# Kernel tuning notes

Measured on AMD Instinct MI355X. Metric: run time of the kernel, lower is better.

## Reference

```python
import jax, jax.numpy as jnp
import numpy as np

N_NODES = 50000
N_EDGES = 800000
H_DIM = 128
N_REL = 40
N_BASES = 4


def setup_inputs() -> dict:
    key = jax.random.key(0)
    ks = jax.random.split(key, 9)
    h = jax.random.normal(ks[0], (N_NODES, H_DIM), jnp.float32)
    norm = jax.random.uniform(ks[1], (N_EDGES, 1), jnp.float32)
    basis_w = jax.random.normal(ks[2], (N_BASES, H_DIM, H_DIM), jnp.float32) * 0.05
    w_comp = jax.random.normal(ks[3], (N_REL, N_BASES), jnp.float32) * 0.5
    loop_w = jax.random.normal(ks[4], (H_DIM, H_DIM), jnp.float32) * 0.05
    bias = jax.random.normal(ks[5], (H_DIM,), jnp.float32) * 0.05
    src = jax.random.randint(ks[6], (N_EDGES,), 0, N_NODES, jnp.int32)
    dst = jax.random.randint(ks[7], (N_EDGES,), 0, N_NODES, jnp.int32)
    etype = jax.random.randint(ks[8], (N_EDGES,), 0, N_REL, jnp.int32)
    return {"h": h, "norm": norm, "basis_w": basis_w, "w_comp": w_comp,
            "loop_w": loop_w, "bias": bias, "src": src, "dst": dst, "etype": etype}


def reference(h, norm, basis_w, w_comp, loop_w, bias, src, dst, etype):
    # RelGraphConv with 'basis' regularizer, one layer (num_hidden_layers=1):
    #   W_r = sum_b w_comp[r, b] * basis_w[b]
    #   m_e = (h[src_e] @ W_{etype_e}) * norm_e
    #   agg[v] = sum_{e: dst_e = v} m_e
    #   out = relu(agg + bias + h @ loop_w)   (dropout = 0)
    # Contraction reordered for memory efficiency: scatter-add per-basis
    # scaled source features first (node-level), then apply small basis GEMMs.
    n = h.shape[0]
    n_bases = basis_w.shape[0]
    coeff = w_comp[etype] * norm          # [E, B] per-edge basis coefficients * norm
    h_src = h[src]                        # [E, D] edge-gathered source features
    agg = jnp.zeros((n, basis_w.shape[2]), dtype=h.dtype)
    for b in range(n_bases):              # small fixed loop over bases
        s_b = jax.ops.segment_sum(coeff[:, b:b + 1] * h_src, dst, num_segments=n)  # [N, D]
        agg = agg + s_b @ basis_w[b]
    return jax.nn.relu(agg + bias + h @ loop_w)
```

## Files before the change

kernel.cpp:

```cpp
#include <hip/hip_runtime.h>
#include <stdint.h>

#define N_NODES 50000
#define N_EDGES 800000
#define H_DIM 128
#define N_REL 40
#define N_BASES 4
#define N_RANGES 196
#define EP_BLOCKS 200
#define EDGES_PER_BLK 4000
#define STAGE_CAP 5120

typedef __attribute__((ext_vector_type(8))) short bf16x8;
typedef __attribute__((ext_vector_type(4))) float f32x4;

__device__ __forceinline__ unsigned short f2bf(float f) {
    unsigned int u = __float_as_uint(f);
    unsigned int r = u + 0x7fffu + ((u >> 16) & 1u);
    return (unsigned short)(r >> 16);
}

__global__ __launch_bounds__(256) void prep_kernel(
        const float* __restrict__ h,
        const float* __restrict__ basis_w, const float* __restrict__ loop_w,
        const int* __restrict__ src, const int* __restrict__ dst,
        const int* __restrict__ etype, const float* __restrict__ norm,
        unsigned short* __restrict__ A, unsigned short* __restrict__ wt3,
        uint2* __restrict__ pkd, int* __restrict__ gcnt) {
    int bid = blockIdx.x;
    if (bid < 3125) {
        int t = bid * 256 + threadIdx.x;
        int row = t >> 4;
        int cb = (t & 15) * 8;
        const float* p = h + (size_t)row * 128 + cb;
        float4 a0 = ((const float4*)p)[0];
        float4 a1 = ((const float4*)p)[1];
        bf16x8 o;
        o[0] = (short)f2bf(a0.x); o[1] = (short)f2bf(a0.y);
        o[2] = (short)f2bf(a0.z); o[3] = (short)f2bf(a0.w);
        o[4] = (short)f2bf(a1.x); o[5] = (short)f2bf(a1.y);
        o[6] = (short)f2bf(a1.z); o[7] = (short)f2bf(a1.w);
        *(bf16x8*)(A + (size_t)row * H_DIM + cb) = o;
    } else if (bid < 3130) {
        int mat = bid - 3125;
        const float* srcm = (mat < 4) ? (basis_w + mat * 16384) : loop_w;
        int koff = (mat < 4) ? (128 + mat * 128) : 0;
        int t = threadIdx.x;
#pragma unroll
        for (int i = 0; i < 16; ++i) {
            int f = t + i * 256;
            int k = f >> 5;
            int j4 = (f & 31) * 4;
            float4 v = ((const float4*)srcm)[f];
            int kg = koff + k;
            int ks = kg >> 5;
            int quad = (kg >> 3) & 3;
            int jj = kg & 7;
            float vv[4] = {v.x, v.y, v.z, v.w};
#pragma unroll
            for (int d = 0; d < 4; ++d) {
                int j = j4 + d;
                int cg = j >> 4;
                int n16 = j & 15;
                wt3[(size_t)((ks * 8 + cg) * 64 + quad * 16 + n16) * 8 + jj] =
                    f2bf(vv[d]);
            }
        }
    } else {
        __shared__ int lhist[N_RANGES];
        int blk = bid - 3130;
        int t = threadIdx.x;
        if (t < N_RANGES) lhist[t] = 0;
        __syncthreads();
        int e0 = blk * EDGES_PER_BLK;
        for (int i = t; i < EDGES_PER_BLK; i += 256) {
            int e = e0 + i;
            int d = dst[e];
            unsigned int nbf = f2bf(norm[e]);
            pkd[e] = make_uint2((unsigned)src[e] | ((unsigned)etype[e] << 20),
                                (unsigned)d | (nbf << 17));
            atomicAdd(&lhist[d >> 8], 1);
        }
        __syncthreads();
        if (t < N_RANGES) gcnt[t * EP_BLOCKS + blk] = lhist[t];
    }
}

__global__ __launch_bounds__(256) void bucket_scan_a(
        const int* __restrict__ gcnt, int* __restrict__ blkbase,
        int* __restrict__ btot, unsigned* __restrict__ sorted_src,
        float4* __restrict__ sorted_cf) {
    __shared__ int wsum[4];
    int r = blockIdx.x;
    int t = threadIdx.x, lane = t & 63, w = t >> 6;
    if (r == 0 && t < 16) {
        sorted_src[N_EDGES + t] = 0u;
        sorted_cf[N_EDGES + t] = make_float4(0.f, 0.f, 0.f, 0.f);
    }
    int x = (t < EP_BLOCKS) ? gcnt[r * EP_BLOCKS + t] : 0;
    int v = x;
#pragma unroll
    for (int d = 1; d < 64; d <<= 1) {
        int y = __shfl_up(v, d);
        if (lane >= d) v += y;
    }
    if (lane == 63) wsum[w] = v;
    __syncthreads();
    int wpre = 0;
    if (w > 0) wpre += wsum[0];
    if (w > 1) wpre += wsum[1];
    if (w > 2) wpre += wsum[2];
    if (t < EP_BLOCKS) blkbase[r * EP_BLOCKS + t] = wpre + v - x;
    if (t == 255) btot[r] = wpre + v;
}

__global__ __launch_bounds__(256) void binscatter(
        const uint2* __restrict__ pkd, const int* __restrict__ blkbase,
        const int* __restrict__ btot, uint2* __restrict__ bucketed) {
    __shared__ int lcur[N_RANGES];
    __shared__ int wsum[4];
    int t = threadIdx.x, lane = t & 63, w = t >> 6;
    int x = (t < N_RANGES) ? btot[t] : 0;
    int v = x;
#pragma unroll
    for (int d = 1; d < 64; d <<= 1) {
        int y = __shfl_up(v, d);
        if (lane >= d) v += y;
    }
    if (lane == 63) wsum[w] = v;
    __syncthreads();
    int wpre = 0;
    if (w > 0) wpre += wsum[0];
    if (w > 1) wpre += wsum[1];
    if (w > 2) wpre += wsum[2];
    if (t < N_RANGES)
        lcur[t] = (wpre + v - x) + blkbase[t * EP_BLOCKS + blockIdx.x];
    __syncthreads();
    int e0 = blockIdx.x * EDGES_PER_BLK;
    for (int i = t; i < EDGES_PER_BLK; i += 256) {
        uint2 p = pkd[e0 + i];
        int r = (p.y & 0x1FFFF) >> 8;
        int pos = atomicAdd(&lcur[r], 1);
        bucketed[pos] = p;
    }
}

__global__ __launch_bounds__(256) void bucket_sort(
        const int* __restrict__ btot, const uint2* __restrict__ bucketed,
        const float* __restrict__ w_comp,
        unsigned* __restrict__ sorted_src, float4* __restrict__ sorted_cf,
        int* __restrict__ offs) {
    __shared__ int hist[256];
    __shared__ int cur[256];
    __shared__ int wsum[4];
    __shared__ int sbeg;
    __shared__ uint2 stage[STAGE_CAP];
    int r = blockIdx.x;
    int t = threadIdx.x, lane = t & 63, w = t >> 6;
    int x = (t < N_RANGES) ? btot[t] : 0;
    int v = x;
#pragma unroll
    for (int d = 1; d < 64; d <<= 1) {
        int y = __shfl_up(v, d);
        if (lane >= d) v += y;
    }
    if (lane == 63) wsum[w] = v;
    hist[t] = 0;
    __syncthreads();
    int wpre = 0;
    if (w > 0) wpre += wsum[0];
    if (w > 1) wpre += wsum[1];
    if (w > 2) wpre += wsum[2];
    if (t == r) sbeg = wpre + v - x;
    __syncthreads();
    int begin = sbeg;
    int end = begin + btot[r];
    int n = end - begin;
    for (int i = begin + t; i < end; i += 256)
        atomicAdd(&hist[bucketed[i].y & 255], 1);
    __syncthreads();
    int x2 = hist[t];
    int v2 = x2;
#pragma unroll
    for (int d = 1; d < 64; d <<= 1) {
        int y = __shfl_up(v2, d);
        if (lane >= d) v2 += y;
    }
    if (lane == 63) wsum[w] = v2;
    __syncthreads();
    int wpre2 = 0;
    if (w > 0) wpre2 += wsum[0];
    if (w > 1) wpre2 += wsum[1];
    if (w > 2) wpre2 += wsum[2];
    int excl_rel = wpre2 + v2 - x2;
    int node = r * 256 + t;
    if (node < N_NODES) offs[node] = begin + excl_rel;
    if (r == N_RANGES - 1 && t == 0) offs[N_NODES] = N_EDGES;
    cur[t] = excl_rel;
    __syncthreads();
    if (n <= STAGE_CAP) {
        for (int i = begin + t; i < end; i += 256) {
            uint2 p = bucketed[i];
            int pos = atomicAdd(&cur[p.y & 255], 1);
            stage[pos] = make_uint2(p.x, (p.y >> 17) << 16);
        }
        __syncthreads();
        for (int i = t; i < n; i += 256) {
            uint2 p = stage[i];
            float nm = __uint_as_float(p.y);
            float4 wc = ((const float4*)w_comp)[p.x >> 20];
            sorted_src[begin + i] = p.x & 0xFFFFF;
            sorted_cf[begin + i] =
                make_float4(wc.x * nm, wc.y * nm, wc.z * nm, wc.w * nm);
        }
    } else {
        for (int i = begin + t; i < end; i += 256) {
            uint2 p = bucketed[i];
            int pos = atomicAdd(&cur[p.y & 255], 1);
            float nm = __uint_as_float((p.y >> 17) << 16);
            float4 wc = ((const float4*)w_comp)[p.x >> 20];
            sorted_src[begin + pos] = p.x & 0xFFFFF;
            sorted_cf[begin + pos] =
                make_float4(wc.x * nm, wc.y * nm, wc.z * nm, wc.w * nm);
        }
    }
}

__global__ __launch_bounds__(512, 8) void agg_gemm(
        const int* __restrict__ offs, const unsigned* __restrict__ ssrc,
        const float4* __restrict__ scf,
        const unsigned short* __restrict__ Ab,
        const unsigned short* __restrict__ wt3,
        const float* __restrict__ bias, float* __restrict__ out) {
    __shared__ __align__(16) unsigned short S[32 * 640];
    int wv = threadIdx.x >> 6;
    int lane = threadIdx.x & 63;
    int nbase = blockIdx.x * 32;
    const unsigned int* Au = (const unsigned int*)Ab;

#pragma unroll
    for (int q = 0; q < 4; ++q) {
        int row = (wv << 2) + q;
        int v = __builtin_amdgcn_readfirstlane(nbase + row);
        float a0l = 0.f, a0h = 0.f, a1l = 0.f, a1h = 0.f;
        float a2l = 0.f, a2h = 0.f, a3l = 0.f, a3h = 0.f;
        unsigned int hb = 0u;
        if (v < N_NODES) {
            hb = Au[(size_t)v * 64 + lane];
            int begin = __builtin_amdgcn_readfirstlane(offs[v]);
            int end   = __builtin_amdgcn_readfirstlane(offs[v + 1]);
            for (int j = begin; j < end; j += 8) {
                int rem = end - j;
                unsigned su[8];
                float4 c[8];
#pragma unroll
                for (int k = 0; k < 8; ++k) su[k] = ssrc[j + k];
#pragma unroll
                for (int k = 0; k < 8; ++k) c[k] = scf[j + k];
                if (rem < 8) {
#pragma unroll
                    for (int k = 0; k < 8; ++k)
                        if (k >= rem) {
                            su[k] = 0u;
                            c[k] = make_float4(0.f, 0.f, 0.f, 0.f);
                        }
                }
                unsigned u[8];
#pragma unroll
                for (int k = 0; k < 8; ++k)
                    u[k] = Au[(size_t)su[k] * 64 + lane];
#pragma unroll
                for (int k = 0; k < 8; ++k) {
                    float lo = __uint_as_float(u[k] << 16);
                    float hi = __uint_as_float(u[k] & 0xffff0000u);
                    a0l += c[k].x * lo; a0h += c[k].x * hi;
                    a1l += c[k].y * lo; a1h += c[k].y * hi;
                    a2l += c[k].z * lo; a2h += c[k].z * hi;
                    a3l += c[k].w * lo; a3h += c[k].w * hi;
                }
            }
        }
        char* rp = (char*)S + row * 1280;
        int swz = (row & 7) << 4;
        *(unsigned int*)(rp + ((lane * 4) ^ swz)) = hb;
        *(unsigned int*)(rp + ((256 + lane * 4) ^ swz)) =
            (unsigned int)f2bf(a0l) | ((unsigned int)f2bf(a0h) << 16);
        *(unsigned int*)(rp + ((512 + lane * 4) ^ swz)) =
            (unsigned int)f2bf(a1l) | ((unsigned int)f2bf(a1h) << 16);
        *(unsigned int*)(rp + ((768 + lane * 4) ^ swz)) =
            (unsigned int)f2bf(a2l) | ((unsigned int)f2bf(a2h) << 16);
        *(unsigned int*)(rp + ((1024 + lane * 4) ^ swz)) =
            (unsigned int)f2bf(a3l) | ((unsigned int)f2bf(a3h) << 16);
    }
    __syncthreads();

    int n16 = lane & 15;
    int quad = lane >> 4;
    f32x4 acc0 = (f32x4)0.f, acc1 = (f32x4)0.f;

    const char* s0p = (const char*)S + n16 * 1280;
    const char* s1p = s0p + 16 * 1280;
    int swz2 = (n16 & 7) << 4;
    const unsigned short* bwp = wt3 + (size_t)wv * 512 + (size_t)lane * 8;

#pragma unroll
    for (int ks = 0; ks < 20; ++ks) {
        int off = (ks * 64 + quad * 16) ^ swz2;
        bf16x8 a0 = *(const bf16x8*)(s0p + off);
        bf16x8 a1 = *(const bf16x8*)(s1p + off);
        bf16x8 b  = *(const bf16x8*)(bwp + (size_t)ks * 4096);
        acc0 = __builtin_amdgcn_mfma_f32_16x16x32_bf16(a0, b, acc0, 0, 0, 0);
        acc1 = __builtin_amdgcn_mfma_f32_16x16x32_bf16(a1, b, acc1, 0, 0, 0);
    }

    int col = (wv << 4) + n16;
    float bv = bias[col];
#pragma unroll
    for (int rg = 0; rg < 4; ++rg) {
        int r0 = nbase + quad * 4 + rg;
        if (r0 < N_NODES)
            out[(size_t)r0 * H_DIM + col] = fmaxf(acc0[rg] + bv, 0.f);
        int r1 = nbase + 16 + quad * 4 + rg;
        if (r1 < N_NODES)
            out[(size_t)r1 * H_DIM + col] = fmaxf(acc1[rg] + bv, 0.f);
    }
}

extern "C" void kernel_launch(void* const* d_in, const int* in_sizes, int n_in,
                              void* d_out, int out_size, void* d_ws, size_t ws_size,
                              hipStream_t stream) {
    const float* h       = (const float*)d_in[0];
    const float* norm    = (const float*)d_in[1];
    const float* basis_w = (const float*)d_in[2];
    const float* w_comp  = (const float*)d_in[3];
    const float* loop_w  = (const float*)d_in[4];
    const float* bias    = (const float*)d_in[5];
    const int*   src     = (const int*)d_in[6];
    const int*   dst     = (const int*)d_in[7];
    const int*   etype   = (const int*)d_in[8];
    float* out = (float*)d_out;

    char* base = (char*)d_ws;
    unsigned short* wt3       = (unsigned short*)(base + 0);
    unsigned short* A         = (unsigned short*)(base + 163840);
    int*            offs      = (int*)(base + 12963840);
    uint2*          pkd       = (uint2*)(base + 13163848);
    uint2*          bucketed  = (uint2*)(base + 19563848);
    float4*         sorted_cf = (float4*)(base + 25963856);
    unsigned*       sorted_src= (unsigned*)(base + 38764112);
    int*            gcnt      = (int*)(base + 41964176);
    int*            blkbase   = (int*)(base + 42120976);
    int*            btot      = (int*)(base + 42277776);

    prep_kernel<<<3330, 256, 0, stream>>>(h, basis_w, loop_w,
                                          src, dst, etype, norm,
                                          A, wt3, pkd, gcnt);
    bucket_scan_a<<<N_RANGES, 256, 0, stream>>>(gcnt, blkbase, btot,
                                                sorted_src, sorted_cf);
    binscatter<<<EP_BLOCKS, 256, 0, stream>>>(pkd, blkbase, btot, bucketed);
    bucket_sort<<<N_RANGES, 256, 0, stream>>>(btot, bucketed, w_comp,
                                              sorted_src, sorted_cf, offs);
    agg_gemm<<<1563, 512, 0, stream>>>(offs, sorted_src, sorted_cf,
                                       A, wt3, bias, out);
}
```

Measured before the change: 172.4 us.

## Make agg_gemm a persistent kernel with atomic tile queue; widen sort blocks

agg_gemm now launches 1024 persistent blocks that pull 32-node tiles from a global atomic counter (reset in bucket_scan_a), instead of one block per tile. The aim is to balance work across uneven node degrees and avoid the tail of the one-shot grid. The edge loop is split into a full-chunk loop and a masked remainder, and the accumulators become packed float2 vectors so the compiler can emit packed FMAs. binscatter and bucket_sort move to 512-thread blocks. In exchange, each tile now costs extra barriers and an atomic, and fewer resident blocks may hide gather latency less well.

Result: slower. 217.0 us (+25.9%).

```diff
diff --git a/kernel.cpp b/kernel.cpp
--- a/kernel.cpp
+++ b/kernel.cpp
@@ -10,9 +10,11 @@
 #define EP_BLOCKS 200
 #define EDGES_PER_BLK 4000
 #define STAGE_CAP 5120
+#define NTILES 1563
 
 typedef __attribute__((ext_vector_type(8))) short bf16x8;
 typedef __attribute__((ext_vector_type(4))) float f32x4;
+typedef __attribute__((ext_vector_type(2))) float f32x2;
 
 __device__ __forceinline__ unsigned short f2bf(float f) {
     unsigned int u = __float_as_uint(f);
@@ -89,7 +91,7 @@
 __global__ __launch_bounds__(256) void bucket_scan_a(
         const int* __restrict__ gcnt, int* __restrict__ blkbase,
         int* __restrict__ btot, unsigned* __restrict__ sorted_src,
-        float4* __restrict__ sorted_cf) {
+        float4* __restrict__ sorted_cf, int* __restrict__ tctr) {
     __shared__ int wsum[4];
     int r = blockIdx.x;
     int t = threadIdx.x, lane = t & 63, w = t >> 6;
@@ -97,6 +99,7 @@
         sorted_src[N_EDGES + t] = 0u;
         sorted_cf[N_EDGES + t] = make_float4(0.f, 0.f, 0.f, 0.f);
     }
+    if (r == 0 && t == 16) tctr[0] = 0;
     int x = (t < EP_BLOCKS) ? gcnt[r * EP_BLOCKS + t] : 0;
     int v = x;
 #pragma unroll
@@ -114,11 +117,11 @@
     if (t == 255) btot[r] = wpre + v;
 }
 
-__global__ __launch_bounds__(256) void binscatter(
+__global__ __launch_bounds__(512) void binscatter(
         const uint2* __restrict__ pkd, const int* __restrict__ blkbase,
         const int* __restrict__ btot, uint2* __restrict__ bucketed) {
     __shared__ int lcur[N_RANGES];
-    __shared__ int wsum[4];
+    __shared__ int wsum[8];
     int t = threadIdx.x, lane = t & 63, w = t >> 6;
     int x = (t < N_RANGES) ? btot[t] : 0;
     int v = x;
@@ -130,14 +133,14 @@
     if (lane == 63) wsum[w] = v;
     __syncthreads();
     int wpre = 0;
-    if (w > 0) wpre += wsum[0];
-    if (w > 1) wpre += wsum[1];
-    if (w > 2) wpre += wsum[2];
+#pragma unroll
+    for (int ww = 0; ww < 7; ++ww)
+        if (w > ww) wpre += wsum[ww];
     if (t < N_RANGES)
         lcur[t] = (wpre + v - x) + blkbase[t * EP_BLOCKS + blockIdx.x];
     __syncthreads();
     int e0 = blockIdx.x * EDGES_PER_BLK;
-    for (int i = t; i < EDGES_PER_BLK; i += 256) {
+    for (int i = t; i < EDGES_PER_BLK; i += 512) {
         uint2 p = pkd[e0 + i];
         int r = (p.y & 0x1FFFF) >> 8;
         int pos = atomicAdd(&lcur[r], 1);
@@ -145,14 +148,14 @@
     }
 }
 
-__global__ __launch_bounds__(256) void bucket_sort(
+__global__ __launch_bounds__(512) void bucket_sort(
         const int* __restrict__ btot, const uint2* __restrict__ bucketed,
         const float* __restrict__ w_comp,
         unsigned* __restrict__ sorted_src, float4* __restrict__ sorted_cf,
         int* __restrict__ offs) {
     __shared__ int hist[256];
     __shared__ int cur[256];
-    __shared__ int wsum[4];
+    __shared__ int wsum[8];
     __shared__ int sbeg;
     __shared__ uint2 stage[STAGE_CAP];
     int r = blockIdx.x;
@@ -165,21 +168,21 @@
         if (lane >= d) v += y;
     }
     if (lane == 63) wsum[w] = v;
-    hist[t] = 0;
+    if (t < 256) hist[t] = 0;
     __syncthreads();
     int wpre = 0;
-    if (w > 0) wpre += wsum[0];
-    if (w > 1) wpre += wsum[1];
-    if (w > 2) wpre += wsum[2];
+#pragma unroll
+    for (int ww = 0; ww < 7; ++ww)
+        if (w > ww) wpre += wsum[ww];
     if (t == r) sbeg = wpre + v - x;
     __syncthreads();
     int begin = sbeg;
     int end = begin + btot[r];
     int n = end - begin;
-    for (int i = begin + t; i < end; i += 256)
+    for (int i = begin + t; i < end; i += 512)
         atomicAdd(&hist[bucketed[i].y & 255], 1);
     __syncthreads();
-    int x2 = hist[t];
+    int x2 = (t < 256) ? hist[t] : 0;
     int v2 = x2;
 #pragma unroll
     for (int d = 1; d < 64; d <<= 1) {
@@ -189,23 +192,25 @@
     if (lane == 63) wsum[w] = v2;
     __syncthreads();
     int wpre2 = 0;
-    if (w > 0) wpre2 += wsum[0];
-    if (w > 1) wpre2 += wsum[1];
-    if (w > 2) wpre2 += wsum[2];
-    int excl_rel = wpre2 + v2 - x2;
-    int node = r * 256 + t;
-    if (node < N_NODES) offs[node] = begin + excl_rel;
+#pragma unroll
+    for (int ww = 0; ww < 3; ++ww)
+        if (w > ww) wpre2 += wsum[ww];
+    if (t < 256) {
+        int excl_rel = wpre2 + v2 - x2;
+        int node = r * 256 + t;
+        if (node < N_NODES) offs[node] = begin + excl_rel;
+        cur[t] = excl_rel;
+    }
     if (r == N_RANGES - 1 && t == 0) offs[N_NODES] = N_EDGES;
-    cur[t] = excl_rel;
     __syncthreads();
     if (n <= STAGE_CAP) {
-        for (int i = begin + t; i < end; i += 256) {
+        for (int i = begin + t; i < end; i += 512) {
             uint2 p = bucketed[i];
             int pos = atomicAdd(&cur[p.y & 255], 1);
             stage[pos] = make_uint2(p.x, (p.y >> 17) << 16);
         }
         __syncthreads();
-        for (int i = t; i < n; i += 256) {
+        for (int i = t; i < n; i += 512) {
             uint2 p = stage[i];
             float nm = __uint_as_float(p.y);
             float4 wc = ((const float4*)w_comp)[p.x >> 20];
@@ -214,7 +219,7 @@
                 make_float4(wc.x * nm, wc.y * nm, wc.z * nm, wc.w * nm);
         }
     } else {
-        for (int i = begin + t; i < end; i += 256) {
+        for (int i = begin + t; i < end; i += 512) {
             uint2 p = bucketed[i];
             int pos = atomicAdd(&cur[p.y & 255], 1);
             float nm = __uint_as_float((p.y >> 17) << 16);
@@ -231,98 +236,129 @@
         const float4* __restrict__ scf,
         const unsigned short* __restrict__ Ab,
         const unsigned short* __restrict__ wt3,
-        const float* __restrict__ bias, float* __restrict__ out) {
+        const float* __restrict__ bias, float* __restrict__ out,
+        int* __restrict__ tctr) {
     __shared__ __align__(16) unsigned short S[32 * 640];
+    int* stile = (int*)S;
     int wv = threadIdx.x >> 6;
     int lane = threadIdx.x & 63;
-    int nbase = blockIdx.x * 32;
     const unsigned int* Au = (const unsigned int*)Ab;
-
-#pragma unroll
-    for (int q = 0; q < 4; ++q) {
-        int row = (wv << 2) + q;
-        int v = __builtin_amdgcn_readfirstlane(nbase + row);
-        float a0l = 0.f, a0h = 0.f, a1l = 0.f, a1h = 0.f;
-        float a2l = 0.f, a2h = 0.f, a3l = 0.f, a3h = 0.f;
-        unsigned int hb = 0u;
-        if (v < N_NODES) {
-            hb = Au[(size_t)v * 64 + lane];
-            int begin = __builtin_amdgcn_readfirstlane(offs[v]);
-            int end   = __builtin_amdgcn_readfirstlane(offs[v + 1]);
-            for (int j = begin; j < end; j += 8) {
-                int rem = end - j;
-                unsigned su[8];
-                float4 c[8];
-#pragma unroll
-                for (int k = 0; k < 8; ++k) su[k] = ssrc[j + k];
-#pragma unroll
-                for (int k = 0; k < 8; ++k) c[k] = scf[j + k];
-                if (rem < 8) {
+    int n16 = lane & 15;
+    int quad = lane >> 4;
+    const char* s0p = (const char*)S + n16 * 1280;
+    const char* s1p = s0p + 16 * 1280;
+    int swz2 = (n16 & 7) << 4;
+    const unsigned short* bwp = wt3 + (size_t)wv * 512 + (size_t)lane * 8;
+
+    for (;;) {
+        if (threadIdx.x == 0) *stile = atomicAdd(tctr, 1);
+        __syncthreads();
+        int tile = *stile;
+        __syncthreads();
+        if (tile >= NTILES) return;
+        int nbase = tile * 32;
+
+        for (int q = 0; q < 4; ++q) {
+            int row = (wv << 2) + q;
+            int v = __builtin_amdgcn_readfirstlane(nbase + row);
+            f32x2 a0 = 0.f, a1 = 0.f, a2 = 0.f, a3 = 0.f;
+            unsigned int hb = 0u;
+            if (v < N_NODES) {
+                hb = Au[(size_t)v * 64 + lane];
+                int begin = __builtin_amdgcn_readfirstlane(offs[v]);
+                int end   = __builtin_amdgcn_readfirstlane(offs[v + 1]);
+                int cnt = end - begin;
+                int nfull = cnt & ~7;
+                int j = begin;
+                for (; j < begin + nfull; j += 8) {
+                    unsigned su[8];
+                    float4 c[8];
+#pragma unroll
+                    for (int k = 0; k < 8; ++k) su[k] = ssrc[j + k];
+#pragma unroll
+                    for (int k = 0; k < 8; ++k) c[k] = scf[j + k];
+                    unsigned u[8];
+#pragma unroll
+                    for (int k = 0; k < 8; ++k)
+                        u[k] = Au[(size_t)su[k] * 64 + lane];
+#pragma unroll
+                    for (int k = 0; k < 8; ++k) {
+                        f32x2 hv;
+                        hv.x = __uint_as_float(u[k] << 16);
+                        hv.y = __uint_as_float(u[k] & 0xffff0000u);
+                        a0 += hv * c[k].x;
+                        a1 += hv * c[k].y;
+                        a2 += hv * c[k].z;
+                        a3 += hv * c[k].w;
+                    }
+                }
+                int rem = cnt & 7;
+                if (rem) {
+                    unsigned su[8];
+                    float4 c[8];
+#pragma unroll
+                    for (int k = 0; k < 8; ++k) su[k] = ssrc[j + k];
+#pragma unroll
+                    for (int k = 0; k < 8; ++k) c[k] = scf[j + k];
 #pragma unroll
                     for (int k = 0; k < 8; ++k)
                         if (k >= rem) {
                             su[k] = 0u;
                             c[k] = make_float4(0.f, 0.f, 0.f, 0.f);
                         }
-                }
-                unsigned u[8];
-#pragma unroll
-                for (int k = 0; k < 8; ++k)
-                    u[k] = Au[(size_t)su[k] * 64 + lane];
-#pragma unroll
-                for (int k = 0; k < 8; ++k) {
-                    float lo = __uint_as_float(u[k] << 16);
-                    float hi = __uint_as_float(u[k] & 0xffff0000u);
-                    a0l += c[k].x * lo; a0h += c[k].x * hi;
-                    a1l += c[k].y * lo; a1h += c[k].y * hi;
-                    a2l += c[k].z * lo; a2h += c[k].z * hi;
-                    a3l += c[k].w * lo; a3h += c[k].w * hi;
+                    unsigned u[8];
+#pragma unroll
+                    for (int k = 0; k < 8; ++k)
+                        u[k] = Au[(size_t)su[k] * 64 + lane];
+#pragma unroll
+                    for (int k = 0; k < 8; ++k) {
+                        f32x2 hv;
+                        hv.x = __uint_as_float(u[k] << 16);
+                        hv.y = __uint_as_float(u[k] & 0xffff0000u);
+                        a0 += hv * c[k].x;
+                        a1 += hv * c[k].y;
+                        a2 += hv * c[k].z;
+                        a3 += hv * c[k].w;
+                    }
                 }
             }
-        }
-        char* rp = (char*)S + row * 1280;
-        int swz = (row & 7) << 4;
-        *(unsigned int*)(rp + ((lane * 4) ^ swz)) = hb;
-        *(unsigned int*)(rp + ((256 + lane * 4) ^ swz)) =
-            (unsigned int)f2bf(a0l) | ((unsigned int)f2bf(a0h) << 16);
-        *(unsigned int*)(rp + ((512 + lane * 4) ^ swz)) =
-            (unsigned int)f2bf(a1l) | ((unsigned int)f2bf(a1h) << 16);
-        *(unsigned int*)(rp + ((768 + lane * 4) ^ swz)) =
-            (unsigned int)f2bf(a2l) | ((unsigned int)f2bf(a2h) << 16);
-        *(unsigned int*)(rp + ((1024 + lane * 4) ^ swz)) =
-            (unsigned int)f2bf(a3l) | ((unsigned int)f2bf(a3h) << 16);
-    }
-    __syncthreads();
-
-    int n16 = lane & 15;
-    int quad = lane >> 4;
-    f32x4 acc0 = (f32x4)0.f, acc1 = (f32x4)0.f;
-
-    const char* s0p = (const char*)S + n16 * 1280;
-    const char* s1p = s0p + 16 * 1280;
-    int swz2 = (n16 & 7) << 4;
-    const unsigned short* bwp = wt3 + (size_t)wv * 512 + (size_t)lane * 8;
-
-#pragma unroll
-    for (int ks = 0; ks < 20; ++ks) {
-        int off = (ks * 64 + quad * 16) ^ swz2;
-        bf16x8 a0 = *(const bf16x8*)(s0p + off);
-        bf16x8 a1 = *(const bf16x8*)(s1p + off);
-        bf16x8 b  = *(const bf16x8*)(bwp + (size_t)ks * 4096);
-        acc0 = __builtin_amdgcn_mfma_f32_16x16x32_bf16(a0, b, acc0, 0, 0, 0);
-        acc1 = __builtin_amdgcn_mfma_f32_16x16x32_bf16(a1, b, acc1, 0, 0, 0);
-    }
-
-    int col = (wv << 4) + n16;
-    float bv = bias[col];
-#pragma unroll
-    for (int rg = 0; rg < 4; ++rg) {
-        int r0 = nbase + quad * 4 + rg;
-        if (r0 < N_NODES)
-            out[(size_t)r0 * H_DIM + col] = fmaxf(acc0[rg] + bv, 0.f);
-        int r1 = nbase + 16 + quad * 4 + rg;
-        if (r1 < N_NODES)
-            out[(size_t)r1 * H_DIM + col] = fmaxf(acc1[rg] + bv, 0.f);
+            char* rp = (char*)S + row * 1280;
+            int swz = (row & 7) << 4;
+            *(unsigned int*)(rp + ((lane * 4) ^ swz)) = hb;
+            *(unsigned int*)(rp + ((256 + lane * 4) ^ swz)) =
+                (unsigned int)f2bf(a0.x) | ((unsigned int)f2bf(a0.y) << 16);
+            *(unsigned int*)(rp + ((512 + lane * 4) ^ swz)) =
+                (unsigned int)f2bf(a1.x) | ((unsigned int)f2bf(a1.y) << 16);
+            *(unsigned int*)(rp + ((768 + lane * 4) ^ swz)) =
+                (unsigned int)f2bf(a2.x) | ((unsigned int)f2bf(a2.y) << 16);
+            *(unsigned int*)(rp + ((1024 + lane * 4) ^ swz)) =
+                (unsigned int)f2bf(a3.x) | ((unsigned int)f2bf(a3.y) << 16);
+        }
+        __syncthreads();
+
+        f32x4 acc0 = (f32x4)0.f, acc1 = (f32x4)0.f;
+#pragma unroll
+        for (int ks = 0; ks < 20; ++ks) {
+            int off = (ks * 64 + quad * 16) ^ swz2;
+            bf16x8 av0 = *(const bf16x8*)(s0p + off);
+            bf16x8 av1 = *(const bf16x8*)(s1p + off);
+            bf16x8 b   = *(const bf16x8*)(bwp + (size_t)ks * 4096);
+            acc0 = __builtin_amdgcn_mfma_f32_16x16x32_bf16(av0, b, acc0, 0, 0, 0);
+            acc1 = __builtin_amdgcn_mfma_f32_16x16x32_bf16(av1, b, acc1, 0, 0, 0);
+        }
+
+        int col = (wv << 4) + n16;
+        float bv = bias[col];
+#pragma unroll
+        for (int rg = 0; rg < 4; ++rg) {
+            int r0 = nbase + quad * 4 + rg;
+            if (r0 < N_NODES)
+                out[(size_t)r0 * H_DIM + col] = fmaxf(acc0[rg] + bv, 0.f);
+            int r1 = nbase + 16 + quad * 4 + rg;
+            if (r1 < N_NODES)
+                out[(size_t)r1 * H_DIM + col] = fmaxf(acc1[rg] + bv, 0.f);
+        }
+        __syncthreads();
     }
 }
 
@@ -351,15 +387,16 @@
     int*            gcnt      = (int*)(base + 41964176);
     int*            blkbase   = (int*)(base + 42120976);
     int*            btot      = (int*)(base + 42277776);
+    int*            tctr      = (int*)(base + 42278560);
 
     prep_kernel<<<3330, 256, 0, stream>>>(h, basis_w, loop_w,
                                           src, dst, etype, norm,
                                           A, wt3, pkd, gcnt);
     bucket_scan_a<<<N_RANGES, 256, 0, stream>>>(gcnt, blkbase, btot,
-                                                sorted_src, sorted_cf);
-    binscatter<<<EP_BLOCKS, 256, 0, stream>>>(pkd, blkbase, btot, bucketed);
-    bucket_sort<<<N_RANGES, 256, 0, stream>>>(btot, bucketed, w_comp,
+                                                sorted_src, sorted_cf, tctr);
+    binscatter<<<EP_BLOCKS, 512, 0, stream>>>(pkd, blkbase, btot, bucketed);
+    bucket_sort<<<N_RANGES, 512, 0, stream>>>(btot, bucketed, w_comp,
                                               sorted_src, sorted_cf, offs);
-    agg_gemm<<<1563, 512, 0, stream>>>(offs, sorted_src, sorted_cf,
-                                       A, wt3, bias, out);
-}
+    agg_gemm<<<1024, 512, 0, stream>>>(offs, sorted_src, sorted_cf,
+                                       A, wt3, bias, out, tctr);
+}
```
